# Kernel optimization log

Hardware: AMD Instinct MI355X
Metric: run time of the kernel (lower is better)

## Reference

```python
import jax, jax.numpy as jnp
import numpy as np

B = 16384
NUM_ITEMS = 1_000_000
NUM_CATS = 1001  # num_categories + 1
USER_DIM = 64
ITEM_DIM = 64
CAT_DIM = 32  # item_embedding_dim // 2
DIM1 = 10000
DIM2 = 10000
DEEP_IN = USER_DIM + ITEM_DIM + CAT_DIM + 2 + 2  # 164
HID = [128, 64, 32]
BN_EPS = 1e-5


def setup_inputs() -> dict:
    key = jax.random.key(0)
    ks = jax.random.split(key, 24)
    inp = {
        'user_embeddings': jax.random.normal(ks[0], (B, USER_DIM), jnp.float32),
        'price_features': jax.random.normal(ks[1], (B, 2), jnp.float32),
        'temporal_features': jax.random.normal(ks[2], (B, 2), jnp.float32),
        'item_emb': jax.random.normal(ks[3], (NUM_ITEMS, ITEM_DIM), jnp.float32) * 0.02,
        'cat_emb': jax.random.normal(ks[4], (NUM_CATS, CAT_DIM), jnp.float32) * 0.02,
        'wide_emb1': jax.random.normal(ks[5], (DIM1, 1), jnp.float32) * 0.02,
        'wide_emb2': jax.random.normal(ks[6], (DIM2, 1), jnp.float32) * 0.02,
        'cross_W': jax.random.normal(ks[7], (DIM1 * DIM2,), jnp.float32) * 0.001,
        'item_ids': jax.random.randint(ks[8], (B,), 0, NUM_ITEMS),
        'category_ids': jax.random.randint(ks[9], (B,), 0, NUM_CATS),
        'wf1': jax.random.randint(ks[10], (B,), 0, DIM1),
        'wf2': jax.random.randint(ks[11], (B,), 0, DIM2),
    }
    dims = [DEEP_IN] + HID + [1]
    for i in range(4):
        fan_in = dims[i]
        inp[f'W{i+1}'] = jax.random.normal(ks[12 + i], (dims[i], dims[i + 1]), jnp.float32) / np.sqrt(fan_in)
        inp[f'b{i+1}'] = jnp.zeros((dims[i + 1],), jnp.float32)
    for i in range(3):  # batch-norm affine params (eval mode, running stats = 0/1)
        inp[f'g{i+1}'] = jnp.ones((HID[i],), jnp.float32)
        inp[f'be{i+1}'] = jnp.zeros((HID[i],), jnp.float32)
    return inp


def _bn(x, g, b):
    # eval-mode BatchNorm1d with running_mean=0, running_var=1
    return x * (g / jnp.sqrt(1.0 + BN_EPS)) + b


def reference(user_embeddings, price_features, temporal_features, item_emb, cat_emb,
              wide_emb1, wide_emb2, cross_W, W1, b1, W2, b2, W3, b3, W4, b4,
              g1, be1, g2, be2, g3, be3, item_ids, category_ids, wf1, wf2):
    # deep component
    x = jnp.concatenate([user_embeddings, item_emb[item_ids], cat_emb[category_ids],
                         price_features, temporal_features], axis=-1)  # [B, 164]
    x = jax.nn.relu(_bn(x @ W1 + b1, g1, be1))
    x = jax.nn.relu(_bn(x @ W2 + b2, g2, be2))
    x = jax.nn.relu(_bn(x @ W3 + b3, g3, be3))
    deep_out = x @ W4 + b4  # [B, 1]
    # wide component: per-feature 1-d embeddings + cross term.
    # one_hot(f1) outer one_hot(f2) flattened then dotted with cross_W is exactly
    # a gather at flat index f1*DIM2 + f2 (same math, no [B, DIM1*DIM2] intermediate).
    wide_out = wide_emb1[wf1] + wide_emb2[wf2]  # [B, 1]
    flat_idx = wf1 * DIM2 + wf2
    wide_out = wide_out + cross_W[flat_idx][:, None]
    return wide_out + deep_out
```

## Files before the change

kernel.cpp:

```cpp
#include <hip/hip_runtime.h>

#define NROWS_PER_BLK 64
#define NTHREADS      512
#define DEEP_IN       164
#define H1            128
#define H2            64
#define H3            32
#define DIM2_C        10000
#define BN_RS         0.99999500003749968750f

#define ARENA_F 14400

__global__ __launch_bounds__(NTHREADS) void wad_fused(
    const float* __restrict__ user, const float* __restrict__ price,
    const float* __restrict__ temporal, const float* __restrict__ item_emb,
    const float* __restrict__ cat_emb, const float* __restrict__ we1,
    const float* __restrict__ we2, const float* __restrict__ crossW,
    const int* __restrict__ item_ids, const int* __restrict__ cat_ids,
    const int* __restrict__ wf1, const int* __restrict__ wf2,
    const float* __restrict__ W1, const float* __restrict__ b1,
    const float* __restrict__ W2, const float* __restrict__ b2,
    const float* __restrict__ W3, const float* __restrict__ b3,
    const float* __restrict__ W4, const float* __restrict__ b4,
    const float* __restrict__ g1, const float* __restrict__ be1,
    const float* __restrict__ g2, const float* __restrict__ be2,
    const float* __restrict__ g3, const float* __restrict__ be3,
    float* __restrict__ out)
{
    __shared__ float arena[ARENA_F];
    float* xs    = arena;
    float* h1s   = arena;
    float* h2s   = arena + 8192;
    float* h3s   = arena + 12288;
    float* wideS = arena + 14336;

    const int tid  = threadIdx.x;
    const int lane = tid & 63;
    const int wave = tid >> 6;
    const int r0   = blockIdx.x * NROWS_PER_BLK;

    const float bn_rs = rsqrtf(1.0f + 1e-5f);

    for (int idx = tid; idx < NROWS_PER_BLK * DEEP_IN; idx += NTHREADS) {
        int r = idx / DEEP_IN;
        int k = idx - r * DEEP_IN;
        int R = r0 + r;
        float v;
        if (k < 64)       v = user[R * 64 + k];
        else if (k < 128) v = item_emb[item_ids[R] * 64 + (k - 64)];
        else if (k < 160) v = cat_emb[cat_ids[R] * 32 + (k - 128)];
        else if (k < 162) v = price[R * 2 + (k - 160)];
        else              v = temporal[R * 2 + (k - 162)];
        xs[idx] = v;
    }
    if (tid < NROWS_PER_BLK) {
        int R = r0 + tid;
        int f1 = wf1[R], f2 = wf2[R];
        wideS[tid] = we1[f1] + we2[f2] + crossW[f1 * DIM2_C + f2];
    }
    __syncthreads();

    const int c0 = __builtin_amdgcn_readfirstlane(wave * 16);
    float acc[16];
#pragma unroll
    for (int n = 0; n < 16; ++n) acc[n] = 0.0f;
    {
        const float* xrow = xs + lane * DEEP_IN;
        for (int kq = 0; kq < DEEP_IN / 4; ++kq) {
            float4 a = *(const float4*)(xrow + kq * 4);
            const float* wbase = W1 + kq * 4 * H1 + c0;
#pragma unroll
            for (int kk = 0; kk < 4; ++kk) {
                float av = ((const float*)&a)[kk];
#pragma unroll
                for (int n = 0; n < 16; ++n) acc[n] += av * wbase[kk * H1 + n];
            }
        }
    }
    __syncthreads();

#pragma unroll
    for (int n = 0; n < 16; n += 4) {
        float4 o;
#pragma unroll
        for (int e = 0; e < 4; ++e) {
            int c = c0 + n + e;
            float z = (acc[n + e] + b1[c]) * (g1[c] * bn_rs) + be1[c];
            ((float*)&o)[e] = fmaxf(z, 0.0f);
        }
        int kc  = (c0 + n) >> 2;
        int kcs = kc ^ (lane & 7);
        *(float4*)(h1s + lane * H1 + kcs * 4) = o;
    }
    __syncthreads();

    const int c02 = __builtin_amdgcn_readfirstlane(wave * 8);
    float acc2[8];
#pragma unroll
    for (int n = 0; n < 8; ++n) acc2[n] = 0.0f;
    for (int kq = 0; kq < H1 / 4; ++kq) {
        int kcs = kq ^ (lane & 7);
        float4 a = *(const float4*)(h1s + lane * H1 + kcs * 4);
        const float* wbase = W2 + kq * 4 * H2 + c02;
#pragma unroll
        for (int kk = 0; kk < 4; ++kk) {
            float av = ((const float*)&a)[kk];
#pragma unroll
            for (int n = 0; n < 8; ++n) acc2[n] += av * wbase[kk * H2 + n];
        }
    }
#pragma unroll
    for (int n = 0; n < 8; n += 4) {
        float4 o;
#pragma unroll
        for (int e = 0; e < 4; ++e) {
            int c = c02 + n + e;
            float z = (acc2[n + e] + b2[c]) * (g2[c] * bn_rs) + be2[c];
            ((float*)&o)[e] = fmaxf(z, 0.0f);
        }
        int kc  = (c02 + n) >> 2;
        int kcs = kc ^ (lane & 7);
        *(float4*)(h2s + lane * H2 + kcs * 4) = o;
    }
    __syncthreads();

    const int c03 = __builtin_amdgcn_readfirstlane(wave * 4);
    float acc3[4];
#pragma unroll
    for (int n = 0; n < 4; ++n) acc3[n] = 0.0f;
    for (int kq = 0; kq < H2 / 4; ++kq) {
        int kcs = kq ^ (lane & 7);
        float4 a = *(const float4*)(h2s + lane * H2 + kcs * 4);
        const float* wbase = W3 + kq * 4 * H3 + c03;
#pragma unroll
        for (int kk = 0; kk < 4; ++kk) {
            float av = ((const float*)&a)[kk];
#pragma unroll
            for (int n = 0; n < 4; ++n) acc3[n] += av * wbase[kk * H3 + n];
        }
    }
    {
        float4 o;
#pragma unroll
        for (int e = 0; e < 4; ++e) {
            int c = c03 + e;
            float z = (acc3[e] + b3[c]) * (g3[c] * bn_rs) + be3[c];
            ((float*)&o)[e] = fmaxf(z, 0.0f);
        }
        int kc  = c03 >> 2;
        int kcs = kc ^ (lane & 7);
        *(float4*)(h3s + lane * H3 + kcs * 4) = o;
    }
    __syncthreads();

    if (tid < NROWS_PER_BLK) {
        int j = tid;
        float s = b4[0];
#pragma unroll
        for (int kq = 0; kq < H3 / 4; ++kq) {
            int kcs = kq ^ (j & 7);
            float4 a = *(const float4*)(h3s + j * H3 + kcs * 4);
#pragma unroll
            for (int e = 0; e < 4; ++e) s += ((const float*)&a)[e] * W4[kq * 4 + e];
        }
        out[r0 + j] = s + wideS[j];
    }
}

extern "C" void kernel_launch(void* const* d_in, const int* in_sizes, int n_in,
                              void* d_out, int out_size, void* d_ws, size_t ws_size,
                              hipStream_t stream) {
    const float* user     = (const float*)d_in[0];
    const float* price    = (const float*)d_in[1];
    const float* temporal = (const float*)d_in[2];
    const float* item_emb = (const float*)d_in[3];
    const float* cat_emb  = (const float*)d_in[4];
    const float* we1      = (const float*)d_in[5];
    const float* we2      = (const float*)d_in[6];
    const float* crossW   = (const float*)d_in[7];
    const int*   item_ids = (const int*)d_in[8];
    const int*   cat_ids  = (const int*)d_in[9];
    const int*   wf1      = (const int*)d_in[10];
    const int*   wf2      = (const int*)d_in[11];
    const float* W1 = (const float*)d_in[12];
    const float* b1 = (const float*)d_in[13];
    const float* W2 = (const float*)d_in[14];
    const float* b2 = (const float*)d_in[15];
    const float* W3 = (const float*)d_in[16];
    const float* b3 = (const float*)d_in[17];
    const float* W4 = (const float*)d_in[18];
    const float* b4 = (const float*)d_in[19];
    const float* g1  = (const float*)d_in[20];
    const float* be1 = (const float*)d_in[21];
    const float* g2  = (const float*)d_in[22];
    const float* be2 = (const float*)d_in[23];
    const float* g3  = (const float*)d_in[24];
    const float* be3 = (const float*)d_in[25];
    float* out = (float*)d_out;

    const int nblocks = 16384 / NROWS_PER_BLK;
    wad_fused<<<nblocks, NTHREADS, 0, stream>>>(
        user, price, temporal, item_emb, cat_emb, we1, we2, crossW,
        item_ids, cat_ids, wf1, wf2,
        W1, b1, W2, b2, W3, b3, W4, b4,
        g1, be1, g2, be2, g3, be3, out);
}
```

Before: 615.1 us.

## Halve rows per block, split columns across half-waves, vectorize gathers and weight loads

Rows per block drop from 64 to 32, so there are twice as many blocks. Each wave now splits its output columns between two half-waves, so each thread computes 8/4/2 outputs per layer instead of 16/8/4. Input gathers use one float4 per thread with a per-row thread group instead of a scalar div/mod loop. Weights are loaded as float4/float2 vectors, and separate LDS regions for x, h1, h2 and h3 remove the sync between layer 1 and its writeback. The aim is more parallelism and occupancy (launch_bounds NT,4) for a kernel dominated by memory latency. The cost is weight loads that are no longer wave-uniform, which adds per-lane global loads.

```diff
diff --git a/kernel.cpp b/kernel.cpp
--- a/kernel.cpp
+++ b/kernel.cpp
@@ -1,17 +1,21 @@
 #include <hip/hip_runtime.h>
 
-#define NROWS_PER_BLK 64
-#define NTHREADS      512
-#define DEEP_IN       164
-#define H1            128
-#define H2            64
-#define H3            32
-#define DIM2_C        10000
-#define BN_RS         0.99999500003749968750f
-
-#define ARENA_F 14400
-
-__global__ __launch_bounds__(NTHREADS) void wad_fused(
+#define RB        32
+#define NT        512
+#define DEEP_IN   164
+#define H1        128
+#define H2        64
+#define H3        32
+#define DIM2_C    10000
+
+#define XS_OFF   0
+#define H1_OFF   5248
+#define H2_OFF   9344
+#define H3_OFF   11392
+#define WIDE_OFF 12416
+#define ARENA_F  12448
+
+__global__ __launch_bounds__(NT, 4) void wad_fused(
     const float* __restrict__ user, const float* __restrict__ price,
     const float* __restrict__ temporal, const float* __restrict__ item_emb,
     const float* __restrict__ cat_emb, const float* __restrict__ we1,
@@ -28,140 +32,149 @@
     float* __restrict__ out)
 {
     __shared__ float arena[ARENA_F];
-    float* xs    = arena;
-    float* h1s   = arena;
-    float* h2s   = arena + 8192;
-    float* h3s   = arena + 12288;
-    float* wideS = arena + 14336;
+    float* xs    = arena + XS_OFF;
+    float* h1    = arena + H1_OFF;
+    float* h2    = arena + H2_OFF;
+    float* h3    = arena + H3_OFF;
+    float* wideS = arena + WIDE_OFF;
 
     const int tid  = threadIdx.x;
     const int lane = tid & 63;
     const int wave = tid >> 6;
-    const int r0   = blockIdx.x * NROWS_PER_BLK;
+    const int r    = lane & 31;
+    const int h    = lane >> 5;
+    const int r0   = blockIdx.x * RB;
 
     const float bn_rs = rsqrtf(1.0f + 1e-5f);
 
-    for (int idx = tid; idx < NROWS_PER_BLK * DEEP_IN; idx += NTHREADS) {
-        int r = idx / DEEP_IN;
-        int k = idx - r * DEEP_IN;
-        int R = r0 + r;
-        float v;
-        if (k < 64)       v = user[R * 64 + k];
-        else if (k < 128) v = item_emb[item_ids[R] * 64 + (k - 64)];
-        else if (k < 160) v = cat_emb[cat_ids[R] * 32 + (k - 128)];
-        else if (k < 162) v = price[R * 2 + (k - 160)];
-        else              v = temporal[R * 2 + (k - 162)];
-        xs[idx] = v;
-    }
-    if (tid < NROWS_PER_BLK) {
+    {
+        int gr = tid >> 4;
+        int q  = tid & 15;
+        int R  = r0 + gr;
+        float4* dst = (float4*)(xs + gr * DEEP_IN);
+        const float4* up = (const float4*)(user + (size_t)R * 64);
+        dst[q] = up[q];
+        int iid = item_ids[R];
+        const float4* ip = (const float4*)(item_emb + (size_t)iid * 64);
+        dst[16 + q] = ip[q];
+        if (q < 8) {
+            int cid = cat_ids[R];
+            dst[32 + q] = ((const float4*)(cat_emb + (size_t)cid * 32))[q];
+        } else if (q == 8) {
+            float2 p  = *(const float2*)(price + (size_t)R * 2);
+            float2 t2 = *(const float2*)(temporal + (size_t)R * 2);
+            dst[40] = make_float4(p.x, p.y, t2.x, t2.y);
+        }
+    }
+    if (tid < RB) {
         int R = r0 + tid;
         int f1 = wf1[R], f2 = wf2[R];
         wideS[tid] = we1[f1] + we2[f2] + crossW[f1 * DIM2_C + f2];
     }
     __syncthreads();
 
-    const int c0 = __builtin_amdgcn_readfirstlane(wave * 16);
-    float acc[16];
-#pragma unroll
-    for (int n = 0; n < 16; ++n) acc[n] = 0.0f;
-    {
-        const float* xrow = xs + lane * DEEP_IN;
+    {
+        const int c0 = wave * 16 + h * 8;
+        float acc[8];
+#pragma unroll
+        for (int n = 0; n < 8; ++n) acc[n] = 0.0f;
+        const float* xrow  = xs + r * DEEP_IN;
+        const float* wbase = W1 + c0;
+#pragma unroll 2
         for (int kq = 0; kq < DEEP_IN / 4; ++kq) {
             float4 a = *(const float4*)(xrow + kq * 4);
-            const float* wbase = W1 + kq * 4 * H1 + c0;
 #pragma unroll
             for (int kk = 0; kk < 4; ++kk) {
+                const float* wk = wbase + (kq * 4 + kk) * H1;
+                float4 w0 = *(const float4*)(wk);
+                float4 w1 = *(const float4*)(wk + 4);
                 float av = ((const float*)&a)[kk];
-#pragma unroll
-                for (int n = 0; n < 16; ++n) acc[n] += av * wbase[kk * H1 + n];
+                acc[0] += av * w0.x; acc[1] += av * w0.y;
+                acc[2] += av * w0.z; acc[3] += av * w0.w;
+                acc[4] += av * w1.x; acc[5] += av * w1.y;
+                acc[6] += av * w1.z; acc[7] += av * w1.w;
             }
         }
-    }
-    __syncthreads();
-
-#pragma unroll
-    for (int n = 0; n < 16; n += 4) {
+        float4 bb0 = *(const float4*)(b1 + c0), bb1 = *(const float4*)(b1 + c0 + 4);
+        float4 gg0 = *(const float4*)(g1 + c0), gg1 = *(const float4*)(g1 + c0 + 4);
+        float4 ee0 = *(const float4*)(be1 + c0), ee1 = *(const float4*)(be1 + c0 + 4);
+        float4 o0, o1;
+        o0.x = fmaxf((acc[0] + bb0.x) * (gg0.x * bn_rs) + ee0.x, 0.0f);
+        o0.y = fmaxf((acc[1] + bb0.y) * (gg0.y * bn_rs) + ee0.y, 0.0f);
+        o0.z = fmaxf((acc[2] + bb0.z) * (gg0.z * bn_rs) + ee0.z, 0.0f);
+        o0.w = fmaxf((acc[3] + bb0.w) * (gg0.w * bn_rs) + ee0.w, 0.0f);
+        o1.x = fmaxf((acc[4] + bb1.x) * (gg1.x * bn_rs) + ee1.x, 0.0f);
+        o1.y = fmaxf((acc[5] + bb1.y) * (gg1.y * bn_rs) + ee1.y, 0.0f);
+        o1.z = fmaxf((acc[6] + bb1.z) * (gg1.z * bn_rs) + ee1.z, 0.0f);
+        o1.w = fmaxf((acc[7] + bb1.w) * (gg1.w * bn_rs) + ee1.w, 0.0f);
+        int kc = c0 >> 2;
+        *(float4*)(h1 + r * H1 + ((kc    ) ^ (r & 7)) * 4) = o0;
+        *(float4*)(h1 + r * H1 + ((kc + 1) ^ (r & 7)) * 4) = o1;
+    }
+    __syncthreads();
+
+    {
+        const int c2 = wave * 8 + h * 4;
+        float acc2[4];
+#pragma unroll
+        for (int n = 0; n < 4; ++n) acc2[n] = 0.0f;
+#pragma unroll 2
+        for (int kq = 0; kq < H1 / 4; ++kq) {
+            int kcs = kq ^ (r & 7);
+            float4 a = *(const float4*)(h1 + r * H1 + kcs * 4);
+#pragma unroll
+            for (int kk = 0; kk < 4; ++kk) {
+                float4 w = *(const float4*)(W2 + (kq * 4 + kk) * H2 + c2);
+                float av = ((const float*)&a)[kk];
+                acc2[0] += av * w.x; acc2[1] += av * w.y;
+                acc2[2] += av * w.z; acc2[3] += av * w.w;
+            }
+        }
+        float4 bb = *(const float4*)(b2 + c2);
+        float4 gg = *(const float4*)(g2 + c2);
+        float4 ee = *(const float4*)(be2 + c2);
         float4 o;
-#pragma unroll
-        for (int e = 0; e < 4; ++e) {
-            int c = c0 + n + e;
-            float z = (acc[n + e] + b1[c]) * (g1[c] * bn_rs) + be1[c];
-            ((float*)&o)[e] = fmaxf(z, 0.0f);
-        }
-        int kc  = (c0 + n) >> 2;
-        int kcs = kc ^ (lane & 7);
-        *(float4*)(h1s + lane * H1 + kcs * 4) = o;
-    }
-    __syncthreads();
-
-    const int c02 = __builtin_amdgcn_readfirstlane(wave * 8);
-    float acc2[8];
-#pragma unroll
-    for (int n = 0; n < 8; ++n) acc2[n] = 0.0f;
-    for (int kq = 0; kq < H1 / 4; ++kq) {
-        int kcs = kq ^ (lane & 7);
-        float4 a = *(const float4*)(h1s + lane * H1 + kcs * 4);
-        const float* wbase = W2 + kq * 4 * H2 + c02;
-#pragma unroll
-        for (int kk = 0; kk < 4; ++kk) {
-            float av = ((const float*)&a)[kk];
-#pragma unroll
-            for (int n = 0; n < 8; ++n) acc2[n] += av * wbase[kk * H2 + n];
-        }
-    }
-#pragma unroll
-    for (int n = 0; n < 8; n += 4) {
-        float4 o;
-#pragma unroll
-        for (int e = 0; e < 4; ++e) {
-            int c = c02 + n + e;
-            float z = (acc2[n + e] + b2[c]) * (g2[c] * bn_rs) + be2[c];
-            ((float*)&o)[e] = fmaxf(z, 0.0f);
-        }
-        int kc  = (c02 + n) >> 2;
-        int kcs = kc ^ (lane & 7);
-        *(float4*)(h2s + lane * H2 + kcs * 4) = o;
-    }
-    __syncthreads();
-
-    const int c03 = __builtin_amdgcn_readfirstlane(wave * 4);
-    float acc3[4];
-#pragma unroll
-    for (int n = 0; n < 4; ++n) acc3[n] = 0.0f;
-    for (int kq = 0; kq < H2 / 4; ++kq) {
-        int kcs = kq ^ (lane & 7);
-        float4 a = *(const float4*)(h2s + lane * H2 + kcs * 4);
-        const float* wbase = W3 + kq * 4 * H3 + c03;
-#pragma unroll
-        for (int kk = 0; kk < 4; ++kk) {
-            float av = ((const float*)&a)[kk];
-#pragma unroll
-            for (int n = 0; n < 4; ++n) acc3[n] += av * wbase[kk * H3 + n];
-        }
-    }
-    {
-        float4 o;
-#pragma unroll
-        for (int e = 0; e < 4; ++e) {
-            int c = c03 + e;
-            float z = (acc3[e] + b3[c]) * (g3[c] * bn_rs) + be3[c];
-            ((float*)&o)[e] = fmaxf(z, 0.0f);
-        }
-        int kc  = c03 >> 2;
-        int kcs = kc ^ (lane & 7);
-        *(float4*)(h3s + lane * H3 + kcs * 4) = o;
-    }
-    __syncthreads();
-
-    if (tid < NROWS_PER_BLK) {
+        o.x = fmaxf((acc2[0] + bb.x) * (gg.x * bn_rs) + ee.x, 0.0f);
+        o.y = fmaxf((acc2[1] + bb.y) * (gg.y * bn_rs) + ee.y, 0.0f);
+        o.z = fmaxf((acc2[2] + bb.z) * (gg.z * bn_rs) + ee.z, 0.0f);
+        o.w = fmaxf((acc2[3] + bb.w) * (gg.w * bn_rs) + ee.w, 0.0f);
+        int kc = c2 >> 2;
+        *(float4*)(h2 + r * H2 + (kc ^ (r & 7)) * 4) = o;
+    }
+    __syncthreads();
+
+    {
+        const int c3 = wave * 4 + h * 2;
+        float a0 = 0.0f, a1 = 0.0f;
+#pragma unroll 2
+        for (int kq = 0; kq < H2 / 4; ++kq) {
+            int kcs = kq ^ (r & 7);
+            float4 a = *(const float4*)(h2 + r * H2 + kcs * 4);
+#pragma unroll
+            for (int kk = 0; kk < 4; ++kk) {
+                float2 w = *(const float2*)(W3 + (kq * 4 + kk) * H3 + c3);
+                float av = ((const float*)&a)[kk];
+                a0 += av * w.x; a1 += av * w.y;
+            }
+        }
+        float z0 = fmaxf((a0 + b3[c3])     * (g3[c3]     * bn_rs) + be3[c3],     0.0f);
+        float z1 = fmaxf((a1 + b3[c3 + 1]) * (g3[c3 + 1] * bn_rs) + be3[c3 + 1], 0.0f);
+        float2 o2 = make_float2(z0, z1);
+        *(float2*)(h3 + r * H3 + (wave ^ (r & 7)) * 4 + h * 2) = o2;
+    }
+    __syncthreads();
+
+    if (tid < RB) {
         int j = tid;
         float s = b4[0];
 #pragma unroll
         for (int kq = 0; kq < H3 / 4; ++kq) {
             int kcs = kq ^ (j & 7);
-            float4 a = *(const float4*)(h3s + j * H3 + kcs * 4);
-#pragma unroll
-            for (int e = 0; e < 4; ++e) s += ((const float*)&a)[e] * W4[kq * 4 + e];
+            float4 a = *(const float4*)(h3 + j * H3 + kcs * 4);
+            s += ((const float*)&a)[0] * W4[kq * 4 + 0];
+            s += ((const float*)&a)[1] * W4[kq * 4 + 1];
+            s += ((const float*)&a)[2] * W4[kq * 4 + 2];
+            s += ((const float*)&a)[3] * W4[kq * 4 + 3];
         }
         out[r0 + j] = s + wideS[j];
     }
@@ -198,8 +211,8 @@
     const float* be3 = (const float*)d_in[25];
     float* out = (float*)d_out;
 
-    const int nblocks = 16384 / NROWS_PER_BLK;
-    wad_fused<<<nblocks, NTHREADS, 0, stream>>>(
+    const int nblocks = 16384 / RB;
+    wad_fused<<<nblocks, NT, 0, stream>>>(
         user, price, temporal, item_emb, cat_emb, we1, we2, crossW,
         item_ids, cat_ids, wf1, wf2,
         W1, b1, W2, b2, W3, b3, W4, b4,
```

New measurement: 625.0 us. No clear change (+1.6%).
